# Optimization experiments

Measured on AMD Instinct MI355X. Metric: run time of the kernel, lower is better.

The kernel has to match this reference:

```python
import jax, jax.numpy as jnp
import numpy as np

N_MOD = 2      # len(l_matrix)
N_SUB = 4096   # each l_matrix entry
DIM = 64
K = 20
ALPHA = 3.0
N = N_MOD * N_SUB  # 8192 total nodes


def setup_inputs() -> dict:
    key = jax.random.key(0)
    k1, k2, k3, k4 = jax.random.split(key, 4)
    nmat = N_MOD * N_MOD
    emb1 = 0.1 * jax.random.normal(k1, (nmat, N_SUB, DIM), dtype=jnp.float32)
    emb2 = 0.1 * jax.random.normal(k2, (nmat, N_SUB, DIM), dtype=jnp.float32)
    # __init__ sets w1/w2 to identity, b to zeros; perturb slightly so they matter
    eye = jnp.eye(DIM, dtype=jnp.float32)
    w1 = eye[None] + 0.01 * jax.random.normal(k3, (nmat, DIM, DIM), dtype=jnp.float32)
    w2 = eye[None] + 0.01 * jax.random.normal(k4, (nmat, DIM, DIM), dtype=jnp.float32)
    b1 = jnp.zeros((nmat, DIM), dtype=jnp.float32)
    b2 = jnp.zeros((nmat, DIM), dtype=jnp.float32)
    idx = jnp.arange(N, dtype=jnp.int64) if jax.config.jax_enable_x64 else jnp.arange(N, dtype=jnp.int32)
    return {"idx": idx, "emb1": emb1, "emb2": emb2, "w1": w1, "w2": w2, "b1": b1, "b2": b2}


def reference(idx, emb1, emb2, w1, w2, b1, b2):
    # per-block linear: nodevec = emb @ w + b   (batched over the nmatrix blocks)
    v1 = jnp.einsum('knd,kde->kne', emb1, w1) + b1[:, None, :]   # [nmat, N_SUB, DIM]
    v2 = jnp.einsum('kmd,kde->kme', emb2, w2) + b2[:, None, :]
    # per-block score: relu(tanh(alpha * v1 @ v2^T))
    a = jnp.einsum('kne,kme->knm', v1, v2)                       # [nmat, N_SUB, N_SUB]
    blocks = jax.nn.relu(jnp.tanh(ALPHA * a))
    # assemble full adjacency: block (i,j) at index i*n_mod + j
    adj = blocks.reshape(N_MOD, N_MOD, N_SUB, N_SUB)
    adj = adj.transpose(0, 2, 1, 3).reshape(N, N)                # [N, N]
    # row-wise topk mask (mask=1 at topk positions), adj * mask
    vals, cols = jax.lax.top_k(adj, K)                           # [N, K]
    rows = jnp.arange(N)[:, None]
    out = jnp.zeros_like(adj).at[rows, cols].set(vals)
    return out


if __name__ == "__main__":
    out = reference(**setup_inputs())
    print(out.shape, float(out.sum()))
```

## Files before the change

### kernel.cpp

```cpp
#include <hip/hip_runtime.h>
#include <hip/hip_bf16.h>

#define NSUB 4096
#define DIM 64
#define NROW 8192
#define KTOP 20
#define CAND 64

typedef unsigned long long u64;
typedef __attribute__((ext_vector_type(8))) short bf16x8;
typedef __attribute__((ext_vector_type(4))) float f32x4;

__device__ __forceinline__ unsigned umax(unsigned a, unsigned b) { return a > b ? a : b; }
__device__ __forceinline__ unsigned umin(unsigned a, unsigned b) { return a < b ? a : b; }

__global__ __launch_bounds__(256) void k_compute_v(
        const float* __restrict__ emb1, const float* __restrict__ w1,
        const float* __restrict__ b1,
        const float* __restrict__ emb2, const float* __restrict__ w2,
        const float* __restrict__ b2,
        double* __restrict__ V1d, double* __restrict__ V2d,
        unsigned short* __restrict__ V1b, unsigned short* __restrict__ V2b) {
    __shared__ alignas(16) float embS[64 * 64];
    __shared__ alignas(16) float wS[64 * 64];
    __shared__ float bS[64];

    int bx    = blockIdx.x;
    int which = bx >> 8;
    int rem   = bx & 255;
    int k     = rem >> 6;
    int tile  = rem & 63;
    int n0    = tile * 64;

    const float* emb = which ? emb2 : emb1;
    const float* w   = which ? w2 : w1;
    const float* b   = which ? b2 : b1;
    double* Vd = which ? V2d : V1d;
    unsigned short* Vb = which ? V2b : V1b;

    int tid = threadIdx.x;
    const float* esrc = emb + ((size_t)k * NSUB + n0) * DIM;
    const float* wsrc = w + (size_t)k * DIM * DIM;
    for (int t = tid; t < 64 * 64; t += 256) { embS[t] = esrc[t]; wS[t] = wsrc[t]; }
    if (tid < 64) bS[tid] = b[k * 64 + tid];
    __syncthreads();

    int e    = tid & 63;
    int mrow = tid >> 6;

    double accs[16];
#pragma unroll
    for (int it = 0; it < 16; ++it) accs[it] = (double)bS[e];

    for (int dg = 0; dg < 16; ++dg) {
        double wv[4];
#pragma unroll
        for (int q = 0; q < 4; ++q) wv[q] = (double)wS[(dg * 4 + q) * 64 + e];
#pragma unroll
        for (int it = 0; it < 16; ++it) {
            float4 em = *(const float4*)&embS[(mrow * 16 + it) * 64 + dg * 4];
            accs[it] += (double)em.x * wv[0] + (double)em.y * wv[1]
                      + (double)em.z * wv[2] + (double)em.w * wv[3];
        }
    }

#pragma unroll
    for (int it = 0; it < 16; ++it) {
        size_t o = ((size_t)k * NSUB + n0 + mrow * 16 + it) * DIM + e;
        Vd[o] = accs[it];
        __hip_bfloat16 hv = __float2bfloat16((float)accs[it]);
        Vb[o] = *reinterpret_cast<unsigned short*>(&hv);
    }
}

__global__ __launch_bounds__(256) void k_stage1(const unsigned short* __restrict__ V1b,
                                                const unsigned short* __restrict__ V2b,
                                                unsigned int* __restrict__ S1) {
    int tid = threadIdx.x;
    int l = tid & 63;
    int w = tid >> 6;
    int bx = blockIdx.x;
    int r0 = (bx >> 1) * 16;
    int h  = bx & 1;
    int i  = r0 >> 12;
    int n0 = r0 & (NSUB - 1);
    int kb = 2 * i + h;

    const unsigned short* ap =
        V1b + ((size_t)kb * NSUB + n0 + (l & 15)) * DIM + ((l >> 4) * 8);
    bf16x8 a0 = *(const bf16x8*)ap;
    bf16x8 a1 = *(const bf16x8*)(ap + 32);

    const unsigned short* bbase =
        V2b + ((size_t)kb * NSUB + w * 1024 + (l & 15)) * DIM + ((l >> 4) * 8);

    unsigned m1[4] = {0, 0, 0, 0}, m2[4] = {0, 0, 0, 0};
    int q = l >> 4;

    for (int s = 0; s < 16; ++s) {
#pragma unroll
        for (int t = 0; t < 4; ++t) {
            const unsigned short* bp = bbase + (size_t)(s * 64 + t * 16) * DIM;
            bf16x8 b0 = *(const bf16x8*)bp;
            bf16x8 b1v = *(const bf16x8*)(bp + 32);
            f32x4 acc = {0.f, 0.f, 0.f, 0.f};
            acc = __builtin_amdgcn_mfma_f32_16x16x32_bf16(a0, b0, acc, 0, 0, 0);
            acc = __builtin_amdgcn_mfma_f32_16x16x32_bf16(a1, b1v, acc, 0, 0, 0);
#pragma unroll
            for (int r = 0; r < 4; ++r) {
                unsigned key = __float_as_uint(fmaxf(acc[r], 0.f));
                m2[r] = umax(m2[r], umin(m1[r], key));
                m1[r] = umax(m1[r], key);
            }
        }
        if ((s & 3) == 3) {
#pragma unroll
            for (int st = 1; st <= 8; st <<= 1) {
#pragma unroll
                for (int r = 0; r < 4; ++r) {
                    unsigned o1 = (unsigned)__shfl_xor((int)m1[r], st);
                    unsigned o2 = (unsigned)__shfl_xor((int)m2[r], st);
                    unsigned nm1 = umax(m1[r], o1);
                    unsigned nm2 = umax(umin(m1[r], o1), umax(m2[r], o2));
                    m1[r] = nm1; m2[r] = nm2;
                }
            }
            if ((l & 15) == 0) {
                int gblk = h * 16 + w * 4 + (s >> 2);
#pragma unroll
                for (int r = 0; r < 4; ++r) {
                    int rowg = r0 + q * 4 + r;
                    uint2 v; v.x = m1[r]; v.y = m2[r];
                    *(uint2*)&S1[(size_t)rowg * 64 + gblk * 2] = v;
                }
            }
#pragma unroll
            for (int r = 0; r < 4; ++r) { m1[r] = 0; m2[r] = 0; }
        }
    }
}

__global__ __launch_bounds__(256) void k_thresh(const unsigned int* __restrict__ S1,
                                                float* __restrict__ Lth) {
    int tid = threadIdx.x;
    int l = tid & 63, w = tid >> 6;
    int row = blockIdx.x * 4 + w;
    unsigned key = S1[(size_t)row * 64 + l];
#pragma unroll
    for (int k = 2; k <= 64; k <<= 1) {
#pragma unroll
        for (int j = k >> 1; j > 0; j >>= 1) {
            unsigned other = (unsigned)__shfl_xor((int)key, j);
            int ixj = l ^ j;
            bool up = ((l & k) == 0);
            bool keepMax = ((l > ixj) == up);
            key = keepMax ? umax(key, other) : umin(key, other);
        }
    }
    if (l == 44) Lth[row] = fmaxf(__uint_as_float(key) - 0.006f, 1e-30f);
}

__global__ __launch_bounds__(256) void k_filter(const unsigned short* __restrict__ V1b,
                                                const unsigned short* __restrict__ V2b,
                                                const float* __restrict__ Lth,
                                                unsigned int* __restrict__ cnt,
                                                int* __restrict__ colsG) {
    __shared__ float Lsh[16];
    int tid = threadIdx.x;
    int l = tid & 63;
    int w = tid >> 6;
    int bx = blockIdx.x;
    int r0 = (bx >> 1) * 16;
    int h  = bx & 1;
    int i  = r0 >> 12;
    int n0 = r0 & (NSUB - 1);
    int kb = 2 * i + h;

    if (tid < 16) Lsh[tid] = Lth[r0 + tid];
    __syncthreads();

    const unsigned short* ap =
        V1b + ((size_t)kb * NSUB + n0 + (l & 15)) * DIM + ((l >> 4) * 8);
    bf16x8 a0 = *(const bf16x8*)ap;
    bf16x8 a1 = *(const bf16x8*)(ap + 32);

    const unsigned short* bbase =
        V2b + ((size_t)kb * NSUB + w * 1024 + (l & 15)) * DIM + ((l >> 4) * 8);

    int q = l >> 4;
    float Lr[4];
#pragma unroll
    for (int r = 0; r < 4; ++r) Lr[r] = Lsh[q * 4 + r];

    for (int s = 0; s < 16; ++s) {
#pragma unroll
        for (int t = 0; t < 4; ++t) {
            const unsigned short* bp = bbase + (size_t)(s * 64 + t * 16) * DIM;
            bf16x8 b0 = *(const bf16x8*)bp;
            bf16x8 b1v = *(const bf16x8*)(bp + 32);
            f32x4 acc = {0.f, 0.f, 0.f, 0.f};
            acc = __builtin_amdgcn_mfma_f32_16x16x32_bf16(a0, b0, acc, 0, 0, 0);
            acc = __builtin_amdgcn_mfma_f32_16x16x32_bf16(a1, b1v, acc, 0, 0, 0);
            int c = h * 4096 + w * 1024 + s * 64 + t * 16 + (l & 15);
#pragma unroll
            for (int r = 0; r < 4; ++r) {
                if (acc[r] >= Lr[r]) {
                    int rowg = r0 + q * 4 + r;
                    unsigned pos = atomicAdd(&cnt[rowg], 1u);
                    if (pos < CAND) colsG[(size_t)rowg * CAND + pos] = c;
                }
            }
        }
    }
}

__global__ __launch_bounds__(256) void k_refine(const double* __restrict__ V1d,
                                                const double* __restrict__ V2d,
                                                const unsigned int* __restrict__ cnt,
                                                const int* __restrict__ colsG,
                                                int* __restrict__ outIdx,
                                                float* __restrict__ outVal) {
    int tid = threadIdx.x;
    int l = tid & 63, w = tid >> 6;
    int row = blockIdx.x * 4 + w;
    int i = row >> 12, n = row & (NSUB - 1);

    unsigned cn = cnt[row];
    if (cn > CAND) cn = CAND;
    bool valid = (unsigned)l < cn;
    int c = valid ? colsG[(size_t)row * CAND + l] : 0;
    int k = 2 * i + (c >> 12);
    int m = c & (NSUB - 1);

    const double* v1p = V1d + ((size_t)k * NSUB + n) * DIM;
    const double* v2p = V2d + ((size_t)k * NSUB + m) * DIM;
    double a = 0.0;
    for (int d = 0; d < DIM; ++d) a += v1p[d] * v2p[d];

    double av = a > 0.0 ? a : 0.0;
    u64 key = (((u64)__double_as_longlong(av)) & ~0x1FFFull) | (u64)(8191 - c);
    if (!valid) key = 0;

    int rank = 0;
    for (int jj = 0; jj < 64; ++jj) {
        u64 kj = (u64)__shfl((long long)key, jj);
        rank += (kj > key || (kj == key && jj < l)) ? 1 : 0;
    }
    if (valid && rank < KTOP) {
        float val = (av > 0.0) ? (float)tanh(3.0 * av) : 0.0f;
        outIdx[(size_t)row * KTOP + rank] = c;
        outVal[(size_t)row * KTOP + rank] = val;
    }
}

__global__ __launch_bounds__(256) void k_write(const int* __restrict__ outIdx,
                                               const float* __restrict__ outVal,
                                               float* __restrict__ out) {
    int t = threadIdx.x;
    size_t base = (size_t)blockIdx.x * 4 * NROW;
    float4 z = {0.f, 0.f, 0.f, 0.f};
    float4* o4 = (float4*)(out + base);
#pragma unroll
    for (int it = 0; it < 32; ++it) o4[it * 256 + t] = z;
    __syncthreads();
    if (t < 4 * KTOP) {
        int row = blockIdx.x * 4 + t / KTOP;
        int c = outIdx[(size_t)blockIdx.x * 4 * KTOP + t];
        float v = outVal[(size_t)blockIdx.x * 4 * KTOP + t];
        out[(size_t)row * NROW + c] = v;
    }
}

extern "C" void kernel_launch(void* const* d_in, const int* in_sizes, int n_in,
                              void* d_out, int out_size, void* d_ws, size_t ws_size,
                              hipStream_t stream) {
    const float* emb1 = (const float*)d_in[1];
    const float* emb2 = (const float*)d_in[2];
    const float* w1   = (const float*)d_in[3];
    const float* w2   = (const float*)d_in[4];
    const float* b1   = (const float*)d_in[5];
    const float* b2   = (const float*)d_in[6];
    float* out = (float*)d_out;

    char* p = (char*)d_out;
    double*         V1d   = (double*)p;
    double*         V2d   = (double*)(p + (size_t)8 * 1024 * 1024);
    unsigned short* V1b   = (unsigned short*)(p + (size_t)16 * 1024 * 1024);
    unsigned short* V2b   = (unsigned short*)(p + (size_t)18 * 1024 * 1024);
    unsigned int*   S1    = (unsigned int*)(p + (size_t)20 * 1024 * 1024);
    int*            colsG = (int*)(p + (size_t)22 * 1024 * 1024);

    int*          outIdx = (int*)d_ws;
    float*        outVal = (float*)((char*)d_ws + (size_t)NROW * KTOP * sizeof(int));
    unsigned int* cntp   = (unsigned int*)((char*)d_ws + (size_t)2 * NROW * KTOP * sizeof(int));
    float*        Lth    = (float*)((char*)cntp + (size_t)NROW * sizeof(unsigned int));

    hipLaunchKernelGGL(k_compute_v, dim3(512), dim3(256), 0, stream,
                       emb1, w1, b1, emb2, w2, b2, V1d, V2d, V1b, V2b);
    hipMemsetAsync(cntp, 0, (size_t)NROW * sizeof(unsigned int), stream);
    hipLaunchKernelGGL(k_stage1, dim3(1024), dim3(256), 0, stream, V1b, V2b, S1);
    hipLaunchKernelGGL(k_thresh, dim3(2048), dim3(256), 0, stream, S1, Lth);
    hipLaunchKernelGGL(k_filter, dim3(1024), dim3(256), 0, stream, V1b, V2b, Lth, cntp, colsG);
    hipLaunchKernelGGL(k_refine, dim3(2048), dim3(256), 0, stream,
                       V1d, V2d, cntp, colsG, outIdx, outVal);
    hipLaunchKernelGGL(k_write, dim3(2048), dim3(256), 0, stream,
                       outIdx, outVal, out);
}
```

Baseline: 478.3 us.

## Process 64 rows per block in stage1 and filter to reuse B fragments

After: 526.2 us. +10.0%, slower.

```diff
diff --git a/kernel.cpp b/kernel.cpp
--- a/kernel.cpp
+++ b/kernel.cpp
@@ -80,62 +80,71 @@
     int l = tid & 63;
     int w = tid >> 6;
     int bx = blockIdx.x;
-    int r0 = (bx >> 1) * 16;
+    int r0 = (bx >> 1) * 64;
     int h  = bx & 1;
     int i  = r0 >> 12;
     int n0 = r0 & (NSUB - 1);
     int kb = 2 * i + h;
-
-    const unsigned short* ap =
-        V1b + ((size_t)kb * NSUB + n0 + (l & 15)) * DIM + ((l >> 4) * 8);
-    bf16x8 a0 = *(const bf16x8*)ap;
-    bf16x8 a1 = *(const bf16x8*)(ap + 32);
-
-    const unsigned short* bbase =
-        V2b + ((size_t)kb * NSUB + w * 1024 + (l & 15)) * DIM + ((l >> 4) * 8);
-
-    unsigned m1[4] = {0, 0, 0, 0}, m2[4] = {0, 0, 0, 0};
-    int q = l >> 4;
-
-    for (int s = 0; s < 16; ++s) {
+    int q  = l >> 4;
+
+    bf16x8 a0[4], a1[4];
+#pragma unroll
+    for (int t = 0; t < 4; ++t) {
+        const unsigned short* ap =
+            V1b + ((size_t)kb * NSUB + n0 + t * 16 + (l & 15)) * DIM + (q * 8);
+        a0[t] = *(const bf16x8*)ap;
+        a1[t] = *(const bf16x8*)(ap + 32);
+    }
+
+    const unsigned short* bp =
+        V2b + ((size_t)kb * NSUB + w * 1024 + (l & 15)) * DIM + (q * 8);
+
+    float m1[16], m2[16];
+#pragma unroll
+    for (int sl = 0; sl < 16; ++sl) { m1[sl] = 0.f; m2[sl] = 0.f; }
+
+    for (int s = 0; s < 64; ++s) {
+        bf16x8 b0 = *(const bf16x8*)bp;
+        bf16x8 b1v = *(const bf16x8*)(bp + 32);
+        bp += 16 * DIM;
 #pragma unroll
         for (int t = 0; t < 4; ++t) {
-            const unsigned short* bp = bbase + (size_t)(s * 64 + t * 16) * DIM;
-            bf16x8 b0 = *(const bf16x8*)bp;
-            bf16x8 b1v = *(const bf16x8*)(bp + 32);
             f32x4 acc = {0.f, 0.f, 0.f, 0.f};
-            acc = __builtin_amdgcn_mfma_f32_16x16x32_bf16(a0, b0, acc, 0, 0, 0);
-            acc = __builtin_amdgcn_mfma_f32_16x16x32_bf16(a1, b1v, acc, 0, 0, 0);
+            acc = __builtin_amdgcn_mfma_f32_16x16x32_bf16(a0[t], b0, acc, 0, 0, 0);
+            acc = __builtin_amdgcn_mfma_f32_16x16x32_bf16(a1[t], b1v, acc, 0, 0, 0);
 #pragma unroll
             for (int r = 0; r < 4; ++r) {
-                unsigned key = __float_as_uint(fmaxf(acc[r], 0.f));
-                m2[r] = umax(m2[r], umin(m1[r], key));
-                m1[r] = umax(m1[r], key);
+                int sl = t * 4 + r;
+                float v = acc[r];
+                m2[sl] = __builtin_amdgcn_fmed3f(v, m1[sl], m2[sl]);
+                m1[sl] = fmaxf(m1[sl], v);
             }
         }
-        if ((s & 3) == 3) {
+        if ((s & 15) == 15) {
 #pragma unroll
             for (int st = 1; st <= 8; st <<= 1) {
 #pragma unroll
-                for (int r = 0; r < 4; ++r) {
-                    unsigned o1 = (unsigned)__shfl_xor((int)m1[r], st);
-                    unsigned o2 = (unsigned)__shfl_xor((int)m2[r], st);
-                    unsigned nm1 = umax(m1[r], o1);
-                    unsigned nm2 = umax(umin(m1[r], o1), umax(m2[r], o2));
-                    m1[r] = nm1; m2[r] = nm2;
+                for (int sl = 0; sl < 16; ++sl) {
+                    float o1 = __shfl_xor(m1[sl], st);
+                    float o2 = __shfl_xor(m2[sl], st);
+                    float nm1 = fmaxf(m1[sl], o1);
+                    float nm2 = fmaxf(fminf(m1[sl], o1), fmaxf(m2[sl], o2));
+                    m1[sl] = nm1; m2[sl] = nm2;
                 }
             }
             if ((l & 15) == 0) {
-                int gblk = h * 16 + w * 4 + (s >> 2);
-#pragma unroll
-                for (int r = 0; r < 4; ++r) {
-                    int rowg = r0 + q * 4 + r;
-                    uint2 v; v.x = m1[r]; v.y = m2[r];
-                    *(uint2*)&S1[(size_t)rowg * 64 + gblk * 2] = v;
+                int gblk = h * 16 + w * 4 + (s >> 4);
+#pragma unroll
+                for (int sl = 0; sl < 16; ++sl) {
+                    int rowg = r0 + (sl >> 2) * 16 + q * 4 + (sl & 3);
+                    uint2 vv;
+                    vv.x = __float_as_uint(m1[sl]);
+                    vv.y = __float_as_uint(m2[sl]);
+                    *(uint2*)&S1[(size_t)rowg * 64 + gblk * 2] = vv;
                 }
             }
 #pragma unroll
-            for (int r = 0; r < 4; ++r) { m1[r] = 0; m2[r] = 0; }
+            for (int sl = 0; sl < 16; ++sl) { m1[sl] = 0.f; m2[sl] = 0.f; }
         }
     }
 }
@@ -165,47 +174,53 @@
                                                 const float* __restrict__ Lth,
                                                 unsigned int* __restrict__ cnt,
                                                 int* __restrict__ colsG) {
-    __shared__ float Lsh[16];
+    __shared__ float Lsh[64];
     int tid = threadIdx.x;
     int l = tid & 63;
     int w = tid >> 6;
     int bx = blockIdx.x;
-    int r0 = (bx >> 1) * 16;
+    int r0 = (bx >> 1) * 64;
     int h  = bx & 1;
     int i  = r0 >> 12;
     int n0 = r0 & (NSUB - 1);
     int kb = 2 * i + h;
-
-    if (tid < 16) Lsh[tid] = Lth[r0 + tid];
+    int q  = l >> 4;
+
+    if (tid < 64) Lsh[tid] = Lth[r0 + tid];
     __syncthreads();
 
-    const unsigned short* ap =
-        V1b + ((size_t)kb * NSUB + n0 + (l & 15)) * DIM + ((l >> 4) * 8);
-    bf16x8 a0 = *(const bf16x8*)ap;
-    bf16x8 a1 = *(const bf16x8*)(ap + 32);
-
-    const unsigned short* bbase =
-        V2b + ((size_t)kb * NSUB + w * 1024 + (l & 15)) * DIM + ((l >> 4) * 8);
-
-    int q = l >> 4;
-    float Lr[4];
-#pragma unroll
-    for (int r = 0; r < 4; ++r) Lr[r] = Lsh[q * 4 + r];
-
-    for (int s = 0; s < 16; ++s) {
+    bf16x8 a0[4], a1[4];
+#pragma unroll
+    for (int t = 0; t < 4; ++t) {
+        const unsigned short* ap =
+            V1b + ((size_t)kb * NSUB + n0 + t * 16 + (l & 15)) * DIM + (q * 8);
+        a0[t] = *(const bf16x8*)ap;
+        a1[t] = *(const bf16x8*)(ap + 32);
+    }
+
+    float Lr[16];
+#pragma unroll
+    for (int sl = 0; sl < 16; ++sl)
+        Lr[sl] = Lsh[(sl >> 2) * 16 + q * 4 + (sl & 3)];
+
+    const unsigned short* bp =
+        V2b + ((size_t)kb * NSUB + w * 1024 + (l & 15)) * DIM + (q * 8);
+
+    for (int s = 0; s < 64; ++s) {
+        bf16x8 b0 = *(const bf16x8*)bp;
+        bf16x8 b1v = *(const bf16x8*)(bp + 32);
+        bp += 16 * DIM;
+        int c = h * 4096 + w * 1024 + s * 16 + (l & 15);
 #pragma unroll
         for (int t = 0; t < 4; ++t) {
-            const unsigned short* bp = bbase + (size_t)(s * 64 + t * 16) * DIM;
-            bf16x8 b0 = *(const bf16x8*)bp;
-            bf16x8 b1v = *(const bf16x8*)(bp + 32);
             f32x4 acc = {0.f, 0.f, 0.f, 0.f};
-            acc = __builtin_amdgcn_mfma_f32_16x16x32_bf16(a0, b0, acc, 0, 0, 0);
-            acc = __builtin_amdgcn_mfma_f32_16x16x32_bf16(a1, b1v, acc, 0, 0, 0);
-            int c = h * 4096 + w * 1024 + s * 64 + t * 16 + (l & 15);
+            acc = __builtin_amdgcn_mfma_f32_16x16x32_bf16(a0[t], b0, acc, 0, 0, 0);
+            acc = __builtin_amdgcn_mfma_f32_16x16x32_bf16(a1[t], b1v, acc, 0, 0, 0);
 #pragma unroll
             for (int r = 0; r < 4; ++r) {
-                if (acc[r] >= Lr[r]) {
-                    int rowg = r0 + q * 4 + r;
+                int sl = t * 4 + r;
+                if (acc[r] >= Lr[sl]) {
+                    int rowg = r0 + t * 16 + q * 4 + r;
                     unsigned pos = atomicAdd(&cnt[rowg], 1u);
                     if (pos < CAND) colsG[(size_t)rowg * CAND + pos] = c;
                 }
@@ -298,9 +313,9 @@
     hipLaunchKernelGGL(k_compute_v, dim3(512), dim3(256), 0, stream,
                        emb1, w1, b1, emb2, w2, b2, V1d, V2d, V1b, V2b);
     hipMemsetAsync(cntp, 0, (size_t)NROW * sizeof(unsigned int), stream);
-    hipLaunchKernelGGL(k_stage1, dim3(1024), dim3(256), 0, stream, V1b, V2b, S1);
+    hipLaunchKernelGGL(k_stage1, dim3(256), dim3(256), 0, stream, V1b, V2b, S1);
     hipLaunchKernelGGL(k_thresh, dim3(2048), dim3(256), 0, stream, S1, Lth);
-    hipLaunchKernelGGL(k_filter, dim3(1024), dim3(256), 0, stream, V1b, V2b, Lth, cntp, colsG);
+    hipLaunchKernelGGL(k_filter, dim3(256), dim3(256), 0, stream, V1b, V2b, Lth, cntp, colsG);
     hipLaunchKernelGGL(k_refine, dim3(2048), dim3(256), 0, stream,
                        V1d, V2d, cntp, colsG, outIdx, outVal);
     hipLaunchKernelGGL(k_write, dim3(2048), dim3(256), 0, stream,
```
